# Optimization experiments

Hardware: AMD Instinct MI355X
Metric: run time of the kernel (lower is better)

## Reference

```python
import jax, jax.numpy as jnp
import numpy as np

BOUND = 3.0
MIN_BIN_W = 1e-3
MIN_BIN_H = 1e-3
MIN_DERIV = 1e-3
MIN_LAMBDA = 0.025
EPS = 1e-6


def _calculate_knots(lengths, lower, upper):
    # lengths: [D, K] summing to 1 along last axis -> scaled lengths and knots [D, K+1]
    knots = jnp.cumsum(lengths, axis=-1)
    knots = jnp.pad(knots, [(0, 0)] * (knots.ndim - 1) + [(1, 0)])
    knots = (upper - lower) * knots + lower
    knots = knots.at[..., 0].set(lower)
    knots = knots.at[..., -1].set(upper)
    return knots[..., 1:] - knots[..., :-1], knots


def _spline_forward(x, uw, uh, ud, ul, bound=BOUND):
    K = uw.shape[-1]
    D = uw.shape[0]
    widths = jax.nn.softmax(uw, axis=-1)
    heights = jax.nn.softmax(uh, axis=-1)
    derivatives = jax.nn.softplus(ud)
    lambdas = jax.nn.sigmoid(ul)

    widths = MIN_BIN_W + (1.0 - MIN_BIN_W * K) * widths
    heights = MIN_BIN_H + (1.0 - MIN_BIN_H * K) * heights
    derivatives = MIN_DERIV + derivatives
    lambdas = (1.0 - 2.0 * MIN_LAMBDA) * lambdas + MIN_LAMBDA

    widths, cumwidths = _calculate_knots(widths, -bound, bound)
    heights, cumheights = _calculate_knots(heights, -bound, bound)
    derivatives = jnp.pad(derivatives, [(0, 0), (1, 1)], constant_values=1.0 - MIN_DERIV)
    # torch mutates the searched knot array in-place: last knot gets +eps
    cumwidths = cumwidths.at[..., -1].add(EPS)

    inside = (x >= -bound) & (x <= bound)
    xin = jnp.where(inside, x, 0.0)  # 0.0 is inside the interval; keeps math NaN-free

    # searchsorted via comparison: [B, D, K+1] -> bin index [B, D]
    bin_idx = jnp.sum((xin[..., None] >= cumwidths).astype(jnp.int32), axis=-1) - 1
    bin_idx = jnp.clip(bin_idx, 0, K - 1)

    d_idx = jnp.arange(D)[None, :]  # broadcast over batch
    sel = lambda t: t[d_idx, bin_idx]  # gather [D, K(+1)] -> [B, D]

    iw = sel(widths)
    icw = sel(cumwidths)
    ich = sel(cumheights)
    idelta = sel(heights / widths)
    id0 = sel(derivatives)
    id1 = sel(derivatives[..., 1:])
    ih = sel(heights)
    il = sel(lambdas)

    wa = 1.0
    wb = jnp.sqrt(id0 / id1) * wa
    wc = (il * wa * id0 + (1.0 - il) * wb * id1) / idelta
    ya = ich
    yb = ih + ich
    yc = ((1.0 - il) * wa * ya + il * wb * yb) / ((1.0 - il) * wa + il * wb)

    theta = (xin - icw) / iw
    left = theta <= il
    numerator = jnp.where(left,
                          wa * ya * (il - theta) + wc * yc * theta,
                          wc * yc * (1.0 - theta) + wb * yb * (theta - il))
    denominator = jnp.where(left,
                            wa * (il - theta) + wc * theta,
                            wc * (1.0 - theta) + wb * (theta - il))
    out = numerator / denominator
    return jnp.where(inside, out, x)


def setup_inputs() -> dict:
    key = jax.random.key(0)
    k1, k2, k3, k4, k5 = jax.random.split(key, 5)
    B, D, K = 65536, 256, 8
    return {
        "x": jax.random.normal(k1, (B, D), dtype=jnp.float32),
        "unnormalized_widths": jax.random.normal(k2, (D, K), dtype=jnp.float32),
        "unnormalized_heights": jax.random.normal(k3, (D, K), dtype=jnp.float32),
        "unnormalized_derivatives": jax.random.normal(k4, (D, K - 1), dtype=jnp.float32),
        "unnormalized_lambdas": jax.random.uniform(k5, (D, K), dtype=jnp.float32),
    }


def reference(x, unnormalized_widths, unnormalized_heights, unnormalized_derivatives, unnormalized_lambdas):
    return _spline_forward(x, unnormalized_widths, unnormalized_heights,
                           unnormalized_derivatives, unnormalized_lambdas)
```

## Files before the change

kernel.cpp:

```cpp
#include <hip/hip_runtime.h>
#include <math.h>

#define DD   256
#define KK   8
#define DTILE 64
#define ROWS  128

__global__ void spline_setup(const float* __restrict__ uw, const float* __restrict__ uh,
                             const float* __restrict__ ud, const float* __restrict__ ul,
                             float4* __restrict__ parG, float* __restrict__ bndG) {
    int d = blockIdx.x * blockDim.x + threadIdx.x;
    if (d >= DD) return;
    const float* uwd = uw + d * KK;
    const float* uhd = uh + d * KK;
    const float* udd = ud + d * (KK - 1);
    const float* uld = ul + d * KK;

    float mw = -1e30f, mh = -1e30f;
    for (int k = 0; k < KK; ++k) { mw = fmaxf(mw, uwd[k]); mh = fmaxf(mh, uhd[k]); }
    double sw = 0.0, sh = 0.0;
    for (int k = 0; k < KK; ++k) { sw += (double)expf(uwd[k] - mw); sh += (double)expf(uhd[k] - mh); }
    double invsw = 1.0 / sw, invsh = 1.0 / sh;

    double kx[KK + 1], ky[KK + 1], der[KK + 1], lam[KK];
    double cw = 0.0, ch = 0.0;
    kx[0] = -3.0; ky[0] = -3.0;
    for (int k = 0; k < KK; ++k) {
        double wk = 1e-3 + (1.0 - 1e-3 * KK) * ((double)expf(uwd[k] - mw) * invsw);
        double hk = 1e-3 + (1.0 - 1e-3 * KK) * ((double)expf(uhd[k] - mh) * invsh);
        cw += wk; ch += hk;
        kx[k + 1] = 6.0 * cw - 3.0;
        ky[k + 1] = 6.0 * ch - 3.0;
    }
    kx[KK] = 3.0; ky[KK] = 3.0;
    der[0] = 1.0 - 1e-3; der[KK] = 1.0 - 1e-3;
    for (int k = 0; k < KK - 1; ++k)
        der[k + 1] = 1e-3 + (double)log1pf(expf(udd[k]));
    for (int k = 0; k < KK; ++k)
        lam[k] = 0.025 + 0.95 * (1.0 / (1.0 + (double)expf(-uld[k])));

    for (int k = 0; k < KK; ++k) {
        double wdt = kx[k + 1] - kx[k];
        double hgt = ky[k + 1] - ky[k];
        double d0 = der[k], d1 = der[k + 1], l = lam[k];
        double delta = hgt / wdt;
        double wb = sqrt(d0 / d1);
        double wc = (l * d0 + (1.0 - l) * wb * d1) / delta;
        double ya = ky[k], yb = ky[k] + hgt;
        double wcyc = wc * (((1.0 - l) * ya + l * wb * yb) / ((1.0 - l) + l * wb));
        double wbyb = wb * yb;
        double invw = 1.0 / wdt, icw = kx[k];

        {
            double A = ya * l, P = wcyc - ya, C = l, Q = wc - 1.0;
            double Bp = P * invw, Dp = Q * invw;
            parG[d * 16 + 2 * k] = make_float4((float)(A - Bp * icw), (float)Bp,
                                               (float)(C - Dp * icw), (float)Dp);
        }
        {
            double A = wcyc - wbyb * l, P = wbyb - wcyc, C = wc - wb * l, Q = wb - wc;
            double Bp = P * invw, Dp = Q * invw;
            parG[d * 16 + 2 * k + 1] = make_float4((float)(A - Bp * icw), (float)Bp,
                                                   (float)(C - Dp * icw), (float)Dp);
        }
        if (k > 0) bndG[d * 15 + (2 * k - 1)] = (float)kx[k];
        bndG[d * 15 + (2 * k)]     = (float)(kx[k] + l * wdt);
    }
}

__global__ __launch_bounds__(256, 4)
void spline_main(const float* __restrict__ x, const float4* __restrict__ parG,
                 const float* __restrict__ bndG, float* __restrict__ out, int B) {
    __shared__ float4 s_par[DTILE * 17];
    __shared__ float  s_bnd[DTILE * 15];

    const int tid = threadIdx.x;
    const int dbase = blockIdx.x * DTILE;

    for (int i = tid; i < DTILE * 16; i += 256) {
        int ld = i >> 4, j = i & 15;
        s_par[ld * 17 + j] = parG[(size_t)(dbase + ld) * 16 + j];
    }
    for (int i = tid; i < DTILE * 15; i += 256) {
        s_bnd[i] = bndG[(size_t)dbase * 15 + i];
    }
    __syncthreads();

    const int lane = tid & 63;
    const int w    = tid >> 6;
    const int d    = dbase + lane;
    const size_t rowbase = (size_t)(blockIdx.y * ROWS + w * (ROWS / 4)) * DD + d;
    const float* xp = x + rowbase;
    float*       op = out + rowbase;
    const int pb = lane * 17;

    const float* bl = &s_bnd[lane * 15];
    const float b1 = bl[0],  b2 = bl[1],  b3 = bl[2],  b4 = bl[3];
    const float b5 = bl[4],  b6 = bl[5],  b7 = bl[6],  b8 = bl[7];
    const float b9 = bl[8],  b10 = bl[9], b11 = bl[10], b12 = bl[11];
    const float b13 = bl[12], b14 = bl[13], b15 = bl[14];

    for (int it = 0; it < (ROWS / 4) / 4; ++it) {
        float xv[4];
#pragma unroll
        for (int r = 0; r < 4; ++r) xv[r] = xp[(size_t)(it * 4 + r) * DD];
#pragma unroll
        for (int r = 0; r < 4; ++r) {
            const float xo = xv[r];
            const float xc = fminf(fmaxf(xo, -3.0f), 3.0f);
            const bool c3 = xc >= b8;
            const float m2 = c3 ? b12 : b4;
            const bool c2 = xc >= m2;
            const float m1 = c3 ? (c2 ? b14 : b10) : (c2 ? b6 : b2);
            const bool c1 = xc >= m1;
            const float t01 = c1 ? b3  : b1;
            const float t23 = c1 ? b7  : b5;
            const float t45 = c1 ? b11 : b9;
            const float t67 = c1 ? b15 : b13;
            const float m0 = c3 ? (c2 ? t67 : t45) : (c2 ? t23 : t01);
            const bool c0 = xc >= m0;
            const int j = (c3 ? 8 : 0) + (c2 ? 4 : 0) + (c1 ? 2 : 0) + (c0 ? 1 : 0);

            const float4 p = s_par[pb + j];
            const float num = fmaf(p.y, xc, p.x);
            const float den = fmaf(p.w, xc, p.z);
            const float res = __fdividef(num, den);
            const bool inside = (xo >= -3.0f) && (xo <= 3.0f);
            op[(size_t)(it * 4 + r) * DD] = inside ? res : xo;
        }
    }
}

extern "C" void kernel_launch(void* const* d_in, const int* in_sizes, int n_in,
                              void* d_out, int out_size, void* d_ws, size_t ws_size,
                              hipStream_t stream) {
    const float* x  = (const float*)d_in[0];
    const float* uw = (const float*)d_in[1];
    const float* uh = (const float*)d_in[2];
    const float* ud = (const float*)d_in[3];
    const float* ul = (const float*)d_in[4];
    float* outp = (float*)d_out;

    const int B = in_sizes[0] / DD;

    float4* parG = (float4*)d_ws;
    float*  bndG = (float*)((char*)d_ws + (size_t)DD * 16 * sizeof(float4));

    spline_setup<<<dim3((DD + 63) / 64), dim3(64), 0, stream>>>(uw, uh, ud, ul, parG, bndG);
    spline_main<<<dim3(DD / DTILE, B / ROWS), dim3(256), 0, stream>>>(x, parG, bndG, outp, B);
}
```

Before: 134.0 us.

## Prefetch x rows in double-buffered groups, swizzle LDS params, use nontemporal stores

The main kernel now loads the next group of 8 rows while computing the current group, so global load latency overlaps with compute. Boundary values are read directly from global memory into registers instead of staging them through shared memory. The parameter table in LDS is rotated per lane group to reduce bank conflicts, and outputs use nontemporal stores. The launch bound is raised to 8 blocks per CU, which caps register use per thread and may cause spills given the larger live register set.

```diff
diff --git a/kernel.cpp b/kernel.cpp
--- a/kernel.cpp
+++ b/kernel.cpp
@@ -68,45 +68,48 @@
     }
 }
 
-__global__ __launch_bounds__(256, 4)
+__global__ __launch_bounds__(256, 8)
 void spline_main(const float* __restrict__ x, const float4* __restrict__ parG,
                  const float* __restrict__ bndG, float* __restrict__ out, int B) {
     __shared__ float4 s_par[DTILE * 17];
-    __shared__ float  s_bnd[DTILE * 15];
 
     const int tid = threadIdx.x;
     const int dbase = blockIdx.x * DTILE;
+    const int lane = tid & 63;
+    const int w    = tid >> 6;
+    const int d    = dbase + lane;
+
+    const float* bp = bndG + (size_t)d * 15;
+    const float b1 = bp[0],  b2 = bp[1],  b3 = bp[2],  b4 = bp[3];
+    const float b5 = bp[4],  b6 = bp[5],  b7 = bp[6],  b8 = bp[7];
+    const float b9 = bp[8],  b10 = bp[9], b11 = bp[10], b12 = bp[11];
+    const float b13 = bp[12], b14 = bp[13], b15 = bp[14];
 
     for (int i = tid; i < DTILE * 16; i += 256) {
-        int ld = i >> 4, j = i & 15;
-        s_par[ld * 17 + j] = parG[(size_t)(dbase + ld) * 16 + j];
-    }
-    for (int i = tid; i < DTILE * 15; i += 256) {
-        s_bnd[i] = bndG[(size_t)dbase * 15 + i];
+        int ld = i >> 4, v = i & 15;
+        s_par[ld * 17 + ((v + (ld >> 3)) & 15)] = parG[(size_t)(dbase + ld) * 16 + v];
     }
     __syncthreads();
 
-    const int lane = tid & 63;
-    const int w    = tid >> 6;
-    const int d    = dbase + lane;
     const size_t rowbase = (size_t)(blockIdx.y * ROWS + w * (ROWS / 4)) * DD + d;
     const float* xp = x + rowbase;
     float*       op = out + rowbase;
-    const int pb = lane * 17;
+    const int pb  = lane * 17;
+    const int rot = lane >> 3;
 
-    const float* bl = &s_bnd[lane * 15];
-    const float b1 = bl[0],  b2 = bl[1],  b3 = bl[2],  b4 = bl[3];
-    const float b5 = bl[4],  b6 = bl[5],  b7 = bl[6],  b8 = bl[7];
-    const float b9 = bl[8],  b10 = bl[9], b11 = bl[10], b12 = bl[11];
-    const float b13 = bl[12], b14 = bl[13], b15 = bl[14];
+    float cur[8], nxt[8];
+#pragma unroll
+    for (int r = 0; r < 8; ++r) cur[r] = xp[(size_t)r * DD];
 
-    for (int it = 0; it < (ROWS / 4) / 4; ++it) {
-        float xv[4];
+#pragma unroll 1
+    for (int g = 0; g < 4; ++g) {
+        if (g < 3) {
 #pragma unroll
-        for (int r = 0; r < 4; ++r) xv[r] = xp[(size_t)(it * 4 + r) * DD];
+            for (int r = 0; r < 8; ++r) nxt[r] = xp[(size_t)((g + 1) * 8 + r) * DD];
+        }
 #pragma unroll
-        for (int r = 0; r < 4; ++r) {
-            const float xo = xv[r];
+        for (int r = 0; r < 8; ++r) {
+            const float xo = cur[r];
             const float xc = fminf(fmaxf(xo, -3.0f), 3.0f);
             const bool c3 = xc >= b8;
             const float m2 = c3 ? b12 : b4;
@@ -121,13 +124,15 @@
             const bool c0 = xc >= m0;
             const int j = (c3 ? 8 : 0) + (c2 ? 4 : 0) + (c1 ? 2 : 0) + (c0 ? 1 : 0);
 
-            const float4 p = s_par[pb + j];
+            const float4 p = s_par[pb + ((j + rot) & 15)];
             const float num = fmaf(p.y, xc, p.x);
             const float den = fmaf(p.w, xc, p.z);
             const float res = __fdividef(num, den);
-            const bool inside = (xo >= -3.0f) && (xo <= 3.0f);
-            op[(size_t)(it * 4 + r) * DD] = inside ? res : xo;
+            const float val = (xo == xc) ? res : xo;
+            __builtin_nontemporal_store(val, &op[(size_t)(g * 8 + r) * DD]);
         }
+#pragma unroll
+        for (int r = 0; r < 8; ++r) cur[r] = nxt[r];
     }
 }
 
```

New measurement: 130.6 us. 2.5% less time.
